# Optimization experiments

Measured on AMD Instinct MI355X. Metric: run time of the kernel, lower is better.

The kernel has to match this reference:

```python
import jax, jax.numpy as jnp
import numpy as np

KNN = 16
BN_EPS = 1e-5


def _swiglu(z, w1, w2, w3):
    # SwiGLU applied over the last dim: w2(silu(w1 z) * (w3 z))
    return (jax.nn.silu(z @ w1.T) * (z @ w3.T)) @ w2.T


def setup_inputs() -> dict:
    key = jax.random.key(0)
    ks = jax.random.split(key, 12)
    B, T, D = 1, 2048, 768
    H, N, KD = 4, 25600, 128
    HID_A, HID_S = 44, 1024
    inp = {
        "x": jax.random.normal(ks[0], (B, T, D), jnp.float32),
        "wq": jax.random.normal(ks[1], (H * KD, D), jnp.float32) * (1.0 / np.sqrt(D)),
        "bq": jax.random.normal(ks[2], (H * KD,), jnp.float32) * 0.02,
        "bn_gamma": jnp.ones((H * KD,), jnp.float32),
        "bn_beta": jnp.zeros((H * KD,), jnp.float32),
        "bn_mean": jnp.zeros((H * KD,), jnp.float32),
        "bn_var": jnp.ones((H * KD,), jnp.float32),
        "keys": jax.random.uniform(ks[3], (H, N, KD), jnp.float32, -1.0 / np.sqrt(KD), 1.0 / np.sqrt(KD)),
        "w_down_tab": jax.random.normal(ks[4], (N, 1), jnp.float32) * 0.02,
        "w_up_tab": jax.random.normal(ks[5], (N, 1), jnp.float32) * 0.02,
        "a_w1": jax.random.normal(ks[6], (HID_A, KNN), jnp.float32) * (1.0 / np.sqrt(KNN)),
        "a_w2": jax.random.normal(ks[7], (KNN, HID_A), jnp.float32) * (1.0 / np.sqrt(HID_A)),
        "a_w3": jax.random.normal(ks[8], (HID_A, KNN), jnp.float32) * (1.0 / np.sqrt(KNN)),
        "s_w1": jax.random.normal(ks[9], (HID_S, D), jnp.float32) * (1.0 / np.sqrt(D)),
        "s_w2": jax.random.normal(ks[10], (D, HID_S), jnp.float32) * (1.0 / np.sqrt(HID_S)),
        "s_w3": jax.random.normal(ks[11], (HID_S, D), jnp.float32) * (1.0 / np.sqrt(D)),
    }
    return inp


def reference(x, wq, bq, bn_gamma, bn_beta, bn_mean, bn_var, keys,
              w_down_tab, w_up_tab, a_w1, a_w2, a_w3, s_w1, s_w2, s_w3):
    B, T, D = x.shape
    H, N, KD = keys.shape
    identity = x
    # query projection + BatchNorm1d (inference: running stats)
    q = x.reshape(-1, D) @ wq.T + bq                      # (bs, H*KD)
    q = (q - bn_mean) * jax.lax.rsqrt(bn_var + BN_EPS) * bn_gamma + bn_beta
    q = q.reshape(-1, H, KD)                              # (bs, H, KD)
    # product-key scoring against full key table, per head
    scores = jnp.einsum('bhk,hnk->bhn', q, keys)          # (bs, H, N)
    top_s, top_i = jax.lax.top_k(scores, KNN)             # (bs, H, KNN)
    gates = jax.nn.softmax(top_s, axis=-1)
    idx = top_i.reshape(B, T, H, KNN)
    gates = gates.reshape(B, T, H, KNN)
    # expert_dim == 1: embedding gather yields a scalar per selected expert
    w_down = w_down_tab[idx, 0]                           # (B, T, H, KNN)
    w_up = w_up_tab[idx, 0]                               # (B, T, H, KNN)
    # einsum('btd,bthkd->bthk') with d-broadcast (expert_dim=1 vs D):
    # equals sum_d x[b,t,d] * w_down[b,t,h,k,0]
    xd = jnp.sum(x, axis=-1)[:, :, None, None] * w_down   # (B, T, H, KNN)
    h = _swiglu(xd, a_w1, a_w2, a_w3)                     # (B, T, H, KNN)
    h = h * gates
    # einsum('bthk,bthkd->btd') with d=1 -> (B, T, 1), broadcasts vs (B,T,D)
    comb = jnp.sum(h * w_up, axis=(2, 3))[:, :, None]     # (B, T, 1)
    out = comb + _swiglu(identity, s_w1, s_w2, s_w3)      # (B, T, D)
    return out
```

## Files before the change

### kernel.cpp

```cpp
#include <hip/hip_runtime.h>
#include <hip/hip_bf16.h>
#include <cmath>

#define NEG_INF (-3.402823466e38f)
#define SPLITS 32
#define SPN    800
#define GRP    32
#define NGRP   25

typedef __attribute__((ext_vector_type(8))) short s16x8;
typedef __attribute__((ext_vector_type(4))) float f32x4;

__device__ __forceinline__ unsigned short f2bf(float f) {
    union { float f; unsigned u; } v; v.f = f;
    unsigned u = v.u;
    u += 0x7fffu + ((u >> 16) & 1u);
    return (unsigned short)(u >> 16);
}

__global__ __launch_bounds__(256) void cvt_all_kernel(
        const float* __restrict__ s0, const float* __restrict__ s1,
        const float* __restrict__ s2, const float* __restrict__ s3,
        const float* __restrict__ s4, const float* __restrict__ keys,
        unsigned short* __restrict__ dst) {
    int i = blockIdx.x * 256 + threadIdx.x;
    if (i >= 4358144) return;
    const float* src; int base;
    if      (i < 393216)  { src = s0;   base = 0; }
    else if (i < 491520)  { src = s1;   base = 393216; }
    else if (i < 688128)  { src = s2;   base = 491520; }
    else if (i < 884736)  { src = s3;   base = 688128; }
    else if (i < 1081344) { src = s4;   base = 884736; }
    else                  { src = keys; base = 1081344; }
    float4 f = ((const float4*)src)[i - base];
    ushort4 o;
    o.x = f2bf(f.x); o.y = f2bf(f.y); o.z = f2bf(f.z); o.w = f2bf(f.w);
    ((ushort4*)dst)[i] = o;
}

__global__ __launch_bounds__(256) void row_sum_kernel(
        const float* __restrict__ x, float* __restrict__ sumx) {
    int gw = (blockIdx.x * 256 + threadIdx.x) >> 6;
    int lane = threadIdx.x & 63;
    const float* row = x + (size_t)gw * 768;
    float s = 0.f;
    #pragma unroll
    for (int k = 0; k < 12; ++k) s += row[lane + k * 64];
    #pragma unroll
    for (int off = 32; off > 0; off >>= 1) s += __shfl_down(s, off);
    if (lane == 0) sumx[gw] = s;
}

template <int EPI>
__global__ __launch_bounds__(256) void gemm_nt(
        const unsigned short* __restrict__ A, const unsigned short* __restrict__ W,
        int M, int N, int K,
        float* __restrict__ outF, unsigned short* __restrict__ outB,
        const float* __restrict__ p0, const float* __restrict__ p1,
        const float* __restrict__ p2, const float* __restrict__ p3,
        const float* __restrict__ p4) {
    __shared__ alignas(16) short As[64][72];
    __shared__ alignas(16) short Ws[64][72];
    const int tid = threadIdx.x;
    const int m0 = blockIdx.x * 64, n0 = blockIdx.y * 64;
    const int wv = tid >> 6, lane = tid & 63;
    const int wr = wv >> 1, wc = wv & 1;
    const int lr = lane & 15, lq = lane >> 4;
    f32x4 acc[2][2];
    #pragma unroll
    for (int i = 0; i < 2; ++i)
        #pragma unroll
        for (int j = 0; j < 2; ++j) acc[i][j] = (f32x4){0.f, 0.f, 0.f, 0.f};

    for (int kb = 0; kb < K; kb += 64) {
        #pragma unroll
        for (int it = 0; it < 2; ++it) {
            int chunk = tid + it * 256;
            int row = chunk >> 3, c8 = (chunk & 7) * 8;
            *(s16x8*)&As[row][c8] = *(const s16x8*)(A + (size_t)(m0 + row) * K + kb + c8);
            *(s16x8*)&Ws[row][c8] = *(const s16x8*)(W + (size_t)(n0 + row) * K + kb + c8);
        }
        __syncthreads();
        #pragma unroll
        for (int ks = 0; ks < 2; ++ks) {
            const int k0 = ks * 32 + lq * 8;
            #pragma unroll
            for (int rt = 0; rt < 2; ++rt) {
                s16x8 a = *(const s16x8*)&As[wr * 32 + rt * 16 + lr][k0];
                #pragma unroll
                for (int ct = 0; ct < 2; ++ct) {
                    s16x8 b = *(const s16x8*)&Ws[wc * 32 + ct * 16 + lr][k0];
                    acc[rt][ct] = __builtin_amdgcn_mfma_f32_16x16x32_bf16(a, b, acc[rt][ct], 0, 0, 0);
                }
            }
        }
        __syncthreads();
    }
    #pragma unroll
    for (int rt = 0; rt < 2; ++rt)
        #pragma unroll
        for (int ct = 0; ct < 2; ++ct)
            #pragma unroll
            for (int r = 0; r < 4; ++r) {
                int m = m0 + wr * 32 + rt * 16 + lq * 4 + r;
                int n = n0 + wc * 32 + ct * 16 + lr;
                float v = acc[rt][ct][r];
                if (EPI == 0) {
                    float q = v + p0[n];
                    q = (q - p3[n]) * rsqrtf(p4[n] + 1e-5f) * p1[n] + p2[n];
                    outB[(size_t)m * N + n] = f2bf(q);
                } else {
                    outF[(size_t)m * N + n] = v + p0[m];
                }
            }
}

__global__ __launch_bounds__(256) void gemm_swiglu_kernel(
        const unsigned short* __restrict__ A, const unsigned short* __restrict__ W1,
        const unsigned short* __restrict__ W3, int M, int N, int K,
        unsigned short* __restrict__ outB) {
    __shared__ alignas(16) short As[64][72];
    __shared__ alignas(16) short W1s[64][72];
    __shared__ alignas(16) short W3s[64][72];
    const int tid = threadIdx.x;
    const int m0 = blockIdx.x * 64, n0 = blockIdx.y * 64;
    const int wv = tid >> 6, lane = tid & 63;
    const int wr = wv >> 1, wc = wv & 1;
    const int lr = lane & 15, lq = lane >> 4;
    f32x4 acc1[2][2], acc3[2][2];
    #pragma unroll
    for (int i = 0; i < 2; ++i)
        #pragma unroll
        for (int j = 0; j < 2; ++j) {
            acc1[i][j] = (f32x4){0.f, 0.f, 0.f, 0.f};
            acc3[i][j] = (f32x4){0.f, 0.f, 0.f, 0.f};
        }
    for (int kb = 0; kb < K; kb += 64) {
        #pragma unroll
        for (int it = 0; it < 2; ++it) {
            int chunk = tid + it * 256;
            int row = chunk >> 3, c8 = (chunk & 7) * 8;
            *(s16x8*)&As[row][c8]  = *(const s16x8*)(A  + (size_t)(m0 + row) * K + kb + c8);
            *(s16x8*)&W1s[row][c8] = *(const s16x8*)(W1 + (size_t)(n0 + row) * K + kb + c8);
            *(s16x8*)&W3s[row][c8] = *(const s16x8*)(W3 + (size_t)(n0 + row) * K + kb + c8);
        }
        __syncthreads();
        #pragma unroll
        for (int ks = 0; ks < 2; ++ks) {
            const int k0 = ks * 32 + lq * 8;
            #pragma unroll
            for (int rt = 0; rt < 2; ++rt) {
                s16x8 a = *(const s16x8*)&As[wr * 32 + rt * 16 + lr][k0];
                #pragma unroll
                for (int ct = 0; ct < 2; ++ct) {
                    s16x8 b1 = *(const s16x8*)&W1s[wc * 32 + ct * 16 + lr][k0];
                    s16x8 b3 = *(const s16x8*)&W3s[wc * 32 + ct * 16 + lr][k0];
                    acc1[rt][ct] = __builtin_amdgcn_mfma_f32_16x16x32_bf16(a, b1, acc1[rt][ct], 0, 0, 0);
                    acc3[rt][ct] = __builtin_amdgcn_mfma_f32_16x16x32_bf16(a, b3, acc3[rt][ct], 0, 0, 0);
                }
            }
        }
        __syncthreads();
    }
    #pragma unroll
    for (int rt = 0; rt < 2; ++rt)
        #pragma unroll
        for (int ct = 0; ct < 2; ++ct)
            #pragma unroll
            for (int r = 0; r < 4; ++r) {
                int m = m0 + wr * 32 + rt * 16 + lq * 4 + r;
                int n = n0 + wc * 32 + ct * 16 + lr;
                float u1 = acc1[rt][ct][r], u3 = acc3[rt][ct][r];
                float hv = u1 / (1.f + expf(-u1)) * u3;
                outB[(size_t)m * N + n] = f2bf(hv);
            }
}

template <int PASS>
__global__ __launch_bounds__(256, 4) void score_pass_kernel(
        const unsigned short* __restrict__ Q,
        const unsigned short* __restrict__ Kt,
        float* __restrict__ maxbuf,
        const float* __restrict__ theta,
        int* __restrict__ cnt,
        float2* __restrict__ buf) {
    __shared__ alignas(16) short Ks[2][GRP][136];
    const int b = blockIdx.x;
    const int tile = b >> 7;
    const int hsp = b & 127;
    const int h = hsp >> 5, sp = hsp & 31;
    const int w = threadIdx.x >> 6, lane = threadIdx.x & 63;
    const int lr = lane & 15, lq = lane >> 4;
    const int t0 = tile * 256 + w * 64;
    const int nb0 = sp * SPN;

    s16x8 qf[4][4];
    #pragma unroll
    for (int tt = 0; tt < 4; ++tt) {
        const unsigned short* qp = Q + (size_t)(t0 + tt * 16 + lr) * 512 + h * 128 + lq * 8;
        #pragma unroll
        for (int ks = 0; ks < 4; ++ks) qf[tt][ks] = *(const s16x8*)(qp + ks * 32);
    }

    float runmax[4] = {NEG_INF, NEG_INF, NEG_INF, NEG_INF};
    float th[4];
    if (PASS == 2) {
        #pragma unroll
        for (int tt = 0; tt < 4; ++tt) th[tt] = theta[(t0 + tt * 16 + lr) * 4 + h];
    }

    const int srow = threadIdx.x >> 4;
    const int scol = (threadIdx.x & 15) * 8;
    const unsigned short* kgp =
        Kt + ((size_t)h * 25600 + nb0 + srow) * 128 + scol;

    {
        *(s16x8*)&Ks[0][srow][scol]      = *(const s16x8*)kgp;
        *(s16x8*)&Ks[0][srow + 16][scol] = *(const s16x8*)(kgp + 2048);
    }

    for (int g = 0; g < NGRP; ++g) {
        s16x8 ka0, ka1;
        if (g + 1 < NGRP) {
            const unsigned short* kp = kgp + (size_t)(g + 1) * 4096;
            ka0 = *(const s16x8*)kp;
            ka1 = *(const s16x8*)(kp + 2048);
        }
        __syncthreads();
        const int cb = g & 1;
        #pragma unroll
        for (int st = 0; st < 2; ++st) {
            f32x4 acc[4];
            #pragma unroll
            for (int tt = 0; tt < 4; ++tt) acc[tt] = (f32x4){0.f, 0.f, 0.f, 0.f};
            #pragma unroll
            for (int ks = 0; ks < 4; ++ks) {
                s16x8 ka = *(const s16x8*)&Ks[cb][st * 16 + lr][ks * 32 + lq * 8];
                #pragma unroll
                for (int tt = 0; tt < 4; ++tt)
                    acc[tt] = __builtin_amdgcn_mfma_f32_16x16x32_bf16(ka, qf[tt][ks], acc[tt], 0, 0, 0);
            }
            if (PASS == 1) {
                #pragma unroll
                for (int tt = 0; tt < 4; ++tt) {
                    float m0 = fmaxf(fmaxf(acc[tt][0], acc[tt][1]),
                                     fmaxf(acc[tt][2], acc[tt][3]));
                    runmax[tt] = fmaxf(runmax[tt], m0);
                }
            } else {
                const int nb = nb0 + g * GRP + st * 16;
                #pragma unroll
                for (int tt = 0; tt < 4; ++tt) {
                    float m0 = fmaxf(fmaxf(acc[tt][0], acc[tt][1]),
                                     fmaxf(acc[tt][2], acc[tt][3]));
                    if (m0 >= th[tt]) {
                        int g4 = (t0 + tt * 16 + lr) * 4 + h;
                        #pragma unroll
                        for (int r = 0; r < 4; ++r) {
                            if (acc[tt][r] >= th[tt]) {
                                int n = nb + lq * 4 + r;
                                int pos = atomicAdd(&cnt[g4], 1);
                                if (pos < 64) {
                                    float2 e; e.x = acc[tt][r]; e.y = __int_as_float(n);
                                    buf[(size_t)g4 * 64 + pos] = e;
                                }
                            }
                        }
                    }
                }
            }
        }
        if (g + 1 < NGRP) {
            const int nbuf = cb ^ 1;
            *(s16x8*)&Ks[nbuf][srow][scol]      = ka0;
            *(s16x8*)&Ks[nbuf][srow + 16][scol] = ka1;
        }
    }

    if (PASS == 1) {
        #pragma unroll
        for (int tt = 0; tt < 4; ++tt)
            maxbuf[(size_t)((t0 + tt * 16 + lr) * 4 + h) * 128 + sp * 4 + lq] = runmax[tt];
    }
}

__global__ __launch_bounds__(64) void theta_kernel(
        const float* __restrict__ maxbuf, float* __restrict__ theta) {
    int g = blockIdx.x * 64 + threadIdx.x;
    if (g >= 8192) return;
    const float* mb = maxbuf + (size_t)g * 128;
    float s[16];
    #pragma unroll
    for (int i = 0; i < 16; ++i) s[i] = NEG_INF;
    for (int j = 0; j < 128; ++j) {
        float v = mb[j];
        if (v > s[15]) {
            #pragma unroll
            for (int i = 15; i > 0; --i)
                s[i] = (v > s[i - 1]) ? s[i - 1] : ((v > s[i]) ? v : s[i]);
            s[0] = (v > s[0]) ? v : s[0];
        }
    }
    theta[g] = s[15];
}

__global__ __launch_bounds__(256) void finalize_kernel(
        const int* __restrict__ cnt, const float2* __restrict__ buf,
        const float* __restrict__ sumx,
        const float* __restrict__ wdown, const float* __restrict__ wup,
        const float* __restrict__ aw1, const float* __restrict__ aw2,
        const float* __restrict__ aw3, float* __restrict__ combsum) {
    __shared__ float zsh[4][16];
    __shared__ float wsh[4][16];
    const int wv = threadIdx.x >> 6, lane = threadIdx.x & 63;
    const int g = blockIdx.x * 4 + wv;
    const int t = g >> 2;
    int c = cnt[g]; c = (c > 64) ? 64 : c;

    float v = NEG_INF; int n = 0x7fffffff;
    if (lane < c) {
        float2 e = buf[(size_t)g * 64 + lane];
        v = e.x; n = __float_as_int(e.y);
    }
    int r = 0;
    for (int i = 0; i < c; ++i) {
        float vi = __shfl(v, i);
        int   ni = __shfl(n, i);
        r += ((vi > v) || (vi == v && ni < n)) ? 1 : 0;
    }
    float m = v;
    #pragma unroll
    for (int off = 32; off > 0; off >>= 1) m = fmaxf(m, __shfl_xor(m, off));
    const bool sel = (lane < c) && (r < 16);
    float e = sel ? expf(v - m) : 0.f;
    float den = e;
    #pragma unroll
    for (int off = 32; off > 0; off >>= 1) den += __shfl_xor(den, off);
    if (sel) {
        zsh[wv][r] = sumx[t] * wdown[n];
        wsh[wv][r] = (e / den) * wup[n];
    }
    __syncthreads();
    float contrib = 0.f;
    if (lane < 44) {
        float u1 = 0.f, u3 = 0.f, cj = 0.f;
        #pragma unroll
        for (int k = 0; k < 16; ++k) {
            float zk = zsh[wv][k];
            u1 += zk * aw1[lane * 16 + k];
            u3 += zk * aw3[lane * 16 + k];
            cj += wsh[wv][k] * aw2[k * 44 + lane];
        }
        float gj = u1 / (1.f + expf(-u1)) * u3;
        contrib = gj * cj;
    }
    #pragma unroll
    for (int off = 32; off > 0; off >>= 1) contrib += __shfl_xor(contrib, off);
    if (lane == 0) atomicAdd(&combsum[t], contrib);
}

extern "C" void kernel_launch(void* const* d_in, const int* in_sizes, int n_in,
                              void* d_out, int out_size, void* d_ws, size_t ws_size,
                              hipStream_t stream) {
    const float* x     = (const float*)d_in[0];
    const float* wq    = (const float*)d_in[1];
    const float* bq    = (const float*)d_in[2];
    const float* gamma = (const float*)d_in[3];
    const float* beta  = (const float*)d_in[4];
    const float* mean  = (const float*)d_in[5];
    const float* var   = (const float*)d_in[6];
    const float* keys  = (const float*)d_in[7];
    const float* wdown = (const float*)d_in[8];
    const float* wup   = (const float*)d_in[9];
    const float* aw1   = (const float*)d_in[10];
    const float* aw2   = (const float*)d_in[11];
    const float* aw3   = (const float*)d_in[12];
    const float* sw1   = (const float*)d_in[13];
    const float* sw2   = (const float*)d_in[14];
    const float* sw3   = (const float*)d_in[15];
    float* out = (float*)d_out;

    char* ws = (char*)d_ws;
    unsigned short* x_b    = (unsigned short*)(ws + 0);
    unsigned short* wq_b   = (unsigned short*)(ws + 3145728);
    unsigned short* sw1_b  = (unsigned short*)(ws + 3932160);
    unsigned short* sw3_b  = (unsigned short*)(ws + 5505024);
    unsigned short* sw2_b  = (unsigned short*)(ws + 7077888);
    unsigned short* keys_b = (unsigned short*)(ws + 8650752);
    unsigned short* q_b    = (unsigned short*)(ws + 34865152);
    float* sumx    = (float*)(ws + 36962304);
    float* theta   = (float*)(ws + 36970496);
    float* combsum = (float*)(ws + 37003264);
    int*   cnt     = (int*)  (ws + 37011456);
    char* R1 = ws + 37044224;
    float* maxbuf = (float*)R1;
    float2* buf   = (float2*)R1;
    unsigned short* h_b = (unsigned short*)R1;

    cvt_all_kernel<<<17024, 256, 0, stream>>>(x, wq, sw1, sw3, sw2, keys, x_b);
    row_sum_kernel<<<512, 256, 0, stream>>>(x, sumx);
    hipMemsetAsync(combsum, 0, 40960, stream);

    gemm_nt<0><<<dim3(32, 8), 256, 0, stream>>>(x_b, wq_b, 2048, 512, 768,
                                                nullptr, q_b, bq, gamma, beta, mean, var);
    score_pass_kernel<1><<<1024, 256, 0, stream>>>(q_b, keys_b, maxbuf, nullptr, nullptr, nullptr);
    theta_kernel<<<128, 64, 0, stream>>>(maxbuf, theta);
    score_pass_kernel<2><<<1024, 256, 0, stream>>>(q_b, keys_b, nullptr, theta, cnt, buf);
    finalize_kernel<<<2048, 256, 0, stream>>>(cnt, buf, sumx, wdown, wup, aw1, aw2, aw3, combsum);
    gemm_swiglu_kernel<<<dim3(32, 16), 256, 0, stream>>>(x_b, sw1_b, sw3_b, 2048, 1024, 768, h_b);
    gemm_nt<2><<<dim3(32, 12), 256, 0, stream>>>(h_b, sw2_b, 2048, 768, 1024,
                                                 out, nullptr, combsum,
                                                 nullptr, nullptr, nullptr, nullptr);
}
```

Before: 355.4 us.

## Process 64-key groups per barrier and transpose maxbuf layout for coalesced theta reads

The key-scoring loop now stages 64 key rows per double-buffered LDS step instead of 32. This halves the number of __syncthreads barriers and lets more prefetch loads be in flight per step, with a 32-row tail handled after the loop. The per-split max buffer is also transposed so that theta_kernel threads read consecutive addresses. The larger tile needs a bigger Ks LDS array, which is not visible in the shown code, and more prefetch registers, which could lower occupancy.

Result: slower. 382.9 us (+7.7%).

```diff
diff --git a/kernel.cpp b/kernel.cpp
--- a/kernel.cpp
+++ b/kernel.cpp
@@ -5,8 +5,8 @@
 #define NEG_INF (-3.402823466e38f)
 #define SPLITS 32
 #define SPN    800
-#define GRP    32
-#define NGRP   25
+#define GRP    64
+#define NG64   12
 
 typedef __attribute__((ext_vector_type(8))) short s16x8;
 typedef __attribute__((ext_vector_type(4))) float f32x4;
@@ -214,73 +214,88 @@
     const unsigned short* kgp =
         Kt + ((size_t)h * 25600 + nb0 + srow) * 128 + scol;
 
-    {
-        *(s16x8*)&Ks[0][srow][scol]      = *(const s16x8*)kgp;
-        *(s16x8*)&Ks[0][srow + 16][scol] = *(const s16x8*)(kgp + 2048);
-    }
-
-    for (int g = 0; g < NGRP; ++g) {
-        s16x8 ka0, ka1;
-        if (g + 1 < NGRP) {
-            const unsigned short* kp = kgp + (size_t)(g + 1) * 4096;
-            ka0 = *(const s16x8*)kp;
-            ka1 = *(const s16x8*)(kp + 2048);
-        }
-        __syncthreads();
-        const int cb = g & 1;
-        #pragma unroll
-        for (int st = 0; st < 2; ++st) {
-            f32x4 acc[4];
-            #pragma unroll
-            for (int tt = 0; tt < 4; ++tt) acc[tt] = (f32x4){0.f, 0.f, 0.f, 0.f};
-            #pragma unroll
-            for (int ks = 0; ks < 4; ++ks) {
-                s16x8 ka = *(const s16x8*)&Ks[cb][st * 16 + lr][ks * 32 + lq * 8];
-                #pragma unroll
-                for (int tt = 0; tt < 4; ++tt)
-                    acc[tt] = __builtin_amdgcn_mfma_f32_16x16x32_bf16(ka, qf[tt][ks], acc[tt], 0, 0, 0);
-            }
-            if (PASS == 1) {
-                #pragma unroll
-                for (int tt = 0; tt < 4; ++tt) {
-                    float m0 = fmaxf(fmaxf(acc[tt][0], acc[tt][1]),
-                                     fmaxf(acc[tt][2], acc[tt][3]));
-                    runmax[tt] = fmaxf(runmax[tt], m0);
-                }
-            } else {
-                const int nb = nb0 + g * GRP + st * 16;
-                #pragma unroll
-                for (int tt = 0; tt < 4; ++tt) {
-                    float m0 = fmaxf(fmaxf(acc[tt][0], acc[tt][1]),
-                                     fmaxf(acc[tt][2], acc[tt][3]));
-                    if (m0 >= th[tt]) {
-                        int g4 = (t0 + tt * 16 + lr) * 4 + h;
-                        #pragma unroll
-                        for (int r = 0; r < 4; ++r) {
-                            if (acc[tt][r] >= th[tt]) {
-                                int n = nb + lq * 4 + r;
-                                int pos = atomicAdd(&cnt[g4], 1);
-                                if (pos < 64) {
-                                    float2 e; e.x = acc[tt][r]; e.y = __int_as_float(n);
-                                    buf[(size_t)g4 * 64 + pos] = e;
-                                }
+    auto do_subtile = [&](int cb, int stbase, int nb) {
+        f32x4 acc[4];
+        #pragma unroll
+        for (int tt = 0; tt < 4; ++tt) acc[tt] = (f32x4){0.f, 0.f, 0.f, 0.f};
+        #pragma unroll
+        for (int ks = 0; ks < 4; ++ks) {
+            s16x8 ka = *(const s16x8*)&Ks[cb][stbase + lr][ks * 32 + lq * 8];
+            #pragma unroll
+            for (int tt = 0; tt < 4; ++tt)
+                acc[tt] = __builtin_amdgcn_mfma_f32_16x16x32_bf16(ka, qf[tt][ks], acc[tt], 0, 0, 0);
+        }
+        if (PASS == 1) {
+            #pragma unroll
+            for (int tt = 0; tt < 4; ++tt) {
+                float m0 = fmaxf(fmaxf(acc[tt][0], acc[tt][1]),
+                                 fmaxf(acc[tt][2], acc[tt][3]));
+                runmax[tt] = fmaxf(runmax[tt], m0);
+            }
+        } else {
+            #pragma unroll
+            for (int tt = 0; tt < 4; ++tt) {
+                float m0 = fmaxf(fmaxf(acc[tt][0], acc[tt][1]),
+                                 fmaxf(acc[tt][2], acc[tt][3]));
+                if (m0 >= th[tt]) {
+                    int g4 = (t0 + tt * 16 + lr) * 4 + h;
+                    #pragma unroll
+                    for (int r = 0; r < 4; ++r) {
+                        if (acc[tt][r] >= th[tt]) {
+                            int n = nb + lq * 4 + r;
+                            int pos = atomicAdd(&cnt[g4], 1);
+                            if (pos < 64) {
+                                float2 e; e.x = acc[tt][r]; e.y = __int_as_float(n);
+                                buf[(size_t)g4 * 64 + pos] = e;
                             }
                         }
                     }
                 }
             }
         }
-        if (g + 1 < NGRP) {
-            const int nbuf = cb ^ 1;
-            *(s16x8*)&Ks[nbuf][srow][scol]      = ka0;
-            *(s16x8*)&Ks[nbuf][srow + 16][scol] = ka1;
-        }
-    }
+    };
+
+    {
+        *(s16x8*)&Ks[0][srow][scol]      = *(const s16x8*)kgp;
+        *(s16x8*)&Ks[0][srow + 16][scol] = *(const s16x8*)(kgp + 2048);
+        *(s16x8*)&Ks[0][srow + 32][scol] = *(const s16x8*)(kgp + 4096);
+        *(s16x8*)&Ks[0][srow + 48][scol] = *(const s16x8*)(kgp + 6144);
+    }
+
+    for (int g = 0; g < NG64; ++g) {
+        s16x8 ka0, ka1, ka2, ka3;
+        {
+            const unsigned short* kp = kgp + (size_t)(g + 1) * 8192;
+            ka0 = *(const s16x8*)kp;
+            ka1 = *(const s16x8*)(kp + 2048);
+            if (g < NG64 - 1) {
+                ka2 = *(const s16x8*)(kp + 4096);
+                ka3 = *(const s16x8*)(kp + 6144);
+            }
+        }
+        __syncthreads();
+        const int cb = g & 1;
+        #pragma unroll
+        for (int st = 0; st < 4; ++st)
+            do_subtile(cb, st * 16, nb0 + g * 64 + st * 16);
+        const int nbuf = cb ^ 1;
+        *(s16x8*)&Ks[nbuf][srow][scol]      = ka0;
+        *(s16x8*)&Ks[nbuf][srow + 16][scol] = ka1;
+        if (g < NG64 - 1) {
+            *(s16x8*)&Ks[nbuf][srow + 32][scol] = ka2;
+            *(s16x8*)&Ks[nbuf][srow + 48][scol] = ka3;
+        }
+    }
+
+    __syncthreads();
+    #pragma unroll
+    for (int st = 0; st < 2; ++st)
+        do_subtile(0, st * 16, nb0 + NG64 * 64 + st * 16);
 
     if (PASS == 1) {
         #pragma unroll
         for (int tt = 0; tt < 4; ++tt)
-            maxbuf[(size_t)((t0 + tt * 16 + lr) * 4 + h) * 128 + sp * 4 + lq] = runmax[tt];
+            maxbuf[(size_t)(sp * 4 + lq) * 8192 + (t0 + tt * 16 + lr) * 4 + h] = runmax[tt];
     }
 }
 
@@ -288,12 +303,12 @@
         const float* __restrict__ maxbuf, float* __restrict__ theta) {
     int g = blockIdx.x * 64 + threadIdx.x;
     if (g >= 8192) return;
-    const float* mb = maxbuf + (size_t)g * 128;
+    const float* mb = maxbuf + g;
     float s[16];
     #pragma unroll
     for (int i = 0; i < 16; ++i) s[i] = NEG_INF;
     for (int j = 0; j < 128; ++j) {
-        float v = mb[j];
+        float v = mb[(size_t)j * 8192];
         if (v > s[15]) {
             #pragma unroll
             for (int i = 15; i > 0; --i)
```
